# Performance work log

Hardware: AMD Instinct MI355X
Metric: run time of the kernel (lower is better)

Reference implementation:

```python
import jax, jax.numpy as jnp
import numpy as np

L, N, D = 4, 50000, 64        # lookback, n_nodes, gnn_dim
E = 500000                    # n_edges
HID = 256
LN_EPS = 1e-5


def setup_inputs() -> dict:
    key = jax.random.key(0)
    ks = jax.random.split(key, 8)
    h_all = jax.random.normal(ks[0], (L, N, D), dtype=jnp.float32)
    src = jax.random.randint(ks[1], (E,), 0, N, dtype=jnp.int32)
    dst = jax.random.randint(ks[2], (E,), 0, N, dtype=jnp.int32)
    W1 = jax.random.normal(ks[3], (HID, L * 2 * D), dtype=jnp.float32) * (1.0 / np.sqrt(L * 2 * D))
    b1 = jax.random.normal(ks[4], (HID,), dtype=jnp.float32) * 0.01
    W3 = jax.random.normal(ks[5], (1, HID), dtype=jnp.float32) * (1.0 / np.sqrt(HID))
    b3 = jax.random.normal(ks[6], (1,), dtype=jnp.float32) * 0.01
    gamma2 = jnp.ones((HID,), dtype=jnp.float32)
    beta2 = jnp.zeros((HID,), dtype=jnp.float32)
    return {"h_all": h_all, "src": src, "dst": dst, "W1": W1, "b1": b1,
            "W3": W3, "b3": b3, "gamma2": gamma2, "beta2": beta2}


def reference(h_all, src, dst, W1, b1, W3, b3, gamma2, beta2):
    lb, _, d = h_all.shape
    # importance weights 1..L normalized
    imp = jnp.arange(1, lb + 1, dtype=h_all.dtype)
    imp = imp / imp.sum()
    # per-edge gather of src/dst features for every lookback step: [L, E, 2D]
    hs = h_all[:, src]                                  # [L, E, D]
    hd = h_all[:, dst]                                  # [L, E, D]
    embed = jnp.concatenate([hs, hd], axis=-1) * imp[:, None, None]
    # concat over lookback steps -> [E, L*2D]
    embed = jnp.transpose(embed, (1, 0, 2)).reshape(embed.shape[1], -1)
    # MLP: W1(tanh) -> LayerNorm -> dropout(eval=identity) -> relu -> W3
    x = jnp.tanh(embed) @ W1.T + b1                     # [E, HID]
    mu = jnp.mean(x, axis=-1, keepdims=True)
    var = jnp.var(x, axis=-1, keepdims=True)
    x = (x - mu) * jax.lax.rsqrt(var + LN_EPS) * gamma2 + beta2
    x = jax.nn.relu(x)
    out = x @ W3.T + b3                                 # [E, 1]
    return out[:, 0]
```

## Files before the change

kernel.cpp:

```cpp
#include <hip/hip_runtime.h>
#include <hip/hip_bf16.h>

#define LL 4
#define NN 50000
#define DD 64
#define EE 500000
#define HID 256
#define KDIM 512
#define LN_EPS 1e-5f

typedef __bf16 bf16x8 __attribute__((ext_vector_type(8)));
typedef float f32x16 __attribute__((ext_vector_type(16)));

__device__ __forceinline__ void async16(const void* g, void* l) {
    __builtin_amdgcn_global_load_lds(
        (const __attribute__((address_space(1))) void*)g,
        (__attribute__((address_space(3))) void*)l, 16, 0, 0);
}

__global__ void w2_conv(const float* __restrict__ w1, __bf16* __restrict__ o) {
    int t = blockIdx.x * 256 + threadIdx.x;
    int j  = t & 511;
    int b  = t >> 9;
    int k0 = (b >> 1) * 16 + (b & 1) * 8;
    int r  = j & 255;
    int col = (k0 >> 6) * 128 + ((j >> 8) ? 64 : 0) + (k0 & 63);
    const float4* p = (const float4*)(w1 + r * KDIM + col);
    float4 va = p[0];
    float4 vb = p[1];
    bf16x8 v;
    v[0] = (__bf16)va.x; v[1] = (__bf16)va.y; v[2] = (__bf16)va.z; v[3] = (__bf16)va.w;
    v[4] = (__bf16)vb.x; v[5] = (__bf16)vb.y; v[6] = (__bf16)vb.z; v[7] = (__bf16)vb.w;
    *(bf16x8*)(o + (size_t)t * 8) = v;
}

__global__ __launch_bounds__(256, 4)
void node_proj(const float* __restrict__ h, const __bf16* __restrict__ w2c,
               const float* __restrict__ b1, __bf16* __restrict__ P) {
    __shared__ __align__(16) __bf16 Bs[2][16384];

    const int tid  = threadIdx.x;
    const int wave = tid >> 6;
    const int lane = tid & 63;
    const int h32  = lane >> 5;
    const int c32  = lane & 31;
    const int n00  = blockIdx.x * 128;

    #pragma unroll
    for (int it = 0; it < 8; ++it) {
        int o = it * 2048 + tid * 8;
        async16(w2c + (size_t)(o >> 9) * 4096 + (o & 511), &Bs[0][o]);
    }

    int node = n00 + wave * 32 + c32;
    if (node >= NN) node = NN - 1;
    bf16x8 af[16];
    #pragma unroll
    for (int u = 0; u < 16; ++u) {
        int l = u >> 2;
        float imp = (float)(l + 1) * 0.1f;
        const float* p = h + (size_t)l * (NN * DD) + node * DD
                       + (u & 3) * 16 + h32 * 8;
        float4 va = *(const float4*)p;
        float4 vb = *(const float4*)(p + 4);
        float xv[8] = {va.x, va.y, va.z, va.w, vb.x, vb.y, vb.z, vb.w};
        #pragma unroll
        for (int z = 0; z < 8; ++z) {
            float e2 = __expf(2.0f * (imp * xv[z]));
            af[u][z] = (__bf16)(1.0f - 2.0f / (e2 + 1.0f));
        }
    }

    __syncthreads();

    for (int p = 0; p < 8; ++p) {
        const int bp = p & 1;
        if (p < 7) {
            #pragma unroll
            for (int it = 0; it < 8; ++it) {
                int o = it * 2048 + tid * 8;
                async16(w2c + (size_t)(o >> 9) * 4096 + (p + 1) * 512 + (o & 511),
                        &Bs[bp ^ 1][o]);
            }
        }

        f32x16 acc[2];
        acc[0] = (f32x16)(0.f);
        acc[1] = (f32x16)(0.f);
        #pragma unroll
        for (int u = 0; u < 16; ++u) {
            const __bf16* Bk = &Bs[bp][(u * 2 + h32) * 512 + c32 * 8];
            #pragma unroll
            for (int nt = 0; nt < 2; ++nt) {
                bf16x8 bf = *(const bf16x8*)(Bk + nt * 256);
                acc[nt] = __builtin_amdgcn_mfma_f32_32x32x16_bf16(af[u], bf, acc[nt], 0, 0, 0);
            }
        }

        #pragma unroll
        for (int nt = 0; nt < 2; ++nt) {
            int col = p * 64 + nt * 32 + c32;
            float b1v = (col >= 256) ? b1[col - 256] : 0.f;
            #pragma unroll
            for (int r = 0; r < 16; ++r) {
                int row = (r & 3) + 8 * (r >> 2) + 4 * h32;
                int n = n00 + wave * 32 + row;
                if (n < NN)
                    P[(size_t)n * 512 + col] = (__bf16)(acc[nt][r] + b1v);
            }
        }

        __syncthreads();
    }
}

__global__ __launch_bounds__(256, 3)
void edge_out(const __bf16* __restrict__ P, const int* __restrict__ src,
              const int* __restrict__ dst,
              const float* __restrict__ w3, const float* __restrict__ b3,
              const float* __restrict__ gamma, const float* __restrict__ beta,
              float* __restrict__ out) {
    const int tid = threadIdx.x;
    const int g   = tid >> 4;
    const int j   = tid & 15;

    float gv[16], btv[16], wv[16];
    {
        const float4* pg = (const float4*)(gamma + j * 16);
        const float4* pt = (const float4*)(beta + j * 16);
        const float4* pw = (const float4*)(w3 + j * 16);
        #pragma unroll
        for (int z = 0; z < 4; ++z) {
            float4 vg = pg[z], vt = pt[z], vw = pw[z];
            gv [z*4+0] = vg.x; gv [z*4+1] = vg.y; gv [z*4+2] = vg.z; gv [z*4+3] = vg.w;
            btv[z*4+0] = vt.x; btv[z*4+1] = vt.y; btv[z*4+2] = vt.z; btv[z*4+3] = vt.w;
            wv [z*4+0] = vw.x; wv [z*4+1] = vw.y; wv [z*4+2] = vw.z; wv [z*4+3] = vw.w;
        }
    }
    const float b3v = b3[0];
    const int e0 = blockIdx.x * 128 + g * 8;

    int ep = e0 + (j & 7);
    if (ep >= EE) ep = EE - 1;
    const int sj = src[ep];
    const int dj = dst[ep];

    uint4 s0[3], s1[3], d0[3], d1[3];

    #pragma unroll
    for (int i = 0; i < 2; ++i) {
        int s = __shfl(sj, i, 16);
        int d = __shfl(dj, i, 16);
        const uint4* ps = (const uint4*)(P + (size_t)s * 512 + j * 16);
        const uint4* pd = (const uint4*)(P + (size_t)d * 512 + 256 + j * 16);
        s0[i] = ps[0]; s1[i] = ps[1]; d0[i] = pd[0]; d1[i] = pd[1];
    }

    #pragma unroll
    for (int i = 0; i < 8; ++i) {
        if (i + 2 < 8) {
            const int slot = (i + 2) % 3;
            int s = __shfl(sj, i + 2, 16);
            int d = __shfl(dj, i + 2, 16);
            const uint4* ps = (const uint4*)(P + (size_t)s * 512 + j * 16);
            const uint4* pd = (const uint4*)(P + (size_t)d * 512 + 256 + j * 16);
            s0[slot] = ps[0]; s1[slot] = ps[1]; d0[slot] = pd[0]; d1[slot] = pd[1];
        }
        const int cs = i % 3;
        bf16x8 a0 = __builtin_bit_cast(bf16x8, s0[cs]);
        bf16x8 a1 = __builtin_bit_cast(bf16x8, s1[cs]);
        bf16x8 c0 = __builtin_bit_cast(bf16x8, d0[cs]);
        bf16x8 c1 = __builtin_bit_cast(bf16x8, d1[cs]);
        float x[16];
        #pragma unroll
        for (int z = 0; z < 8; ++z) {
            x[z]     = (float)a0[z] + (float)c0[z];
            x[z + 8] = (float)a1[z] + (float)c1[z];
        }
        float sum = 0.f, sq = 0.f;
        #pragma unroll
        for (int z = 0; z < 16; ++z) {
            sum += x[z];
            sq   = fmaf(x[z], x[z], sq);
        }
        #pragma unroll
        for (int m = 1; m < 16; m <<= 1) {
            sum += __shfl_xor(sum, m);
            sq  += __shfl_xor(sq,  m);
        }
        float mu = sum * (1.0f / 256.0f);
        float rs = rsqrtf(sq * (1.0f / 256.0f) - mu * mu + LN_EPS);
        float dot = 0.f;
        #pragma unroll
        for (int z = 0; z < 16; ++z) {
            float y = fmaxf((x[z] - mu) * rs * gv[z] + btv[z], 0.f);
            dot = fmaf(y, wv[z], dot);
        }
        #pragma unroll
        for (int m = 1; m < 16; m <<= 1) dot += __shfl_xor(dot, m);
        int e = e0 + i;
        if (j == 0 && e < EE) out[e] = dot + b3v;
        cs0: ;
    }

    #pragma unroll
    for (int z = 0; z < 16; ++z)
        asm volatile("" :: "v"(gv[z]), "v"(btv[z]), "v"(wv[z]));
}

extern "C" void kernel_launch(void* const* d_in, const int* in_sizes, int n_in,
                              void* d_out, int out_size, void* d_ws, size_t ws_size,
                              hipStream_t stream) {
    const float* h_all  = (const float*)d_in[0];
    const int*   src    = (const int*)  d_in[1];
    const int*   dst    = (const int*)  d_in[2];
    const float* W1     = (const float*)d_in[3];
    const float* b1     = (const float*)d_in[4];
    const float* W3     = (const float*)d_in[5];
    const float* b3     = (const float*)d_in[6];
    const float* gamma2 = (const float*)d_in[7];
    const float* beta2  = (const float*)d_in[8];
    float* out = (float*)d_out;

    __bf16* w2c = (__bf16*)d_ws;
    __bf16* P   = w2c + 131072;

    w2_conv<<<64, 256, 0, stream>>>(W1, w2c);
    node_proj<<<(NN + 127) / 128, 256, 0, stream>>>(h_all, w2c, b1, P);
    edge_out<<<(EE + 127) / 128, 256, 0, stream>>>(P, src, dst, W3, b3,
                                                   gamma2, beta2, out);
}
```

Baseline: 216.7 us.

## Stage node_proj output through LDS for coalesced 16-byte stores, wider N tiles

The node projection kernel now computes 128 output columns per pass instead of 64, with one 64KB LDS buffer replacing the double buffer. Results are staged in LDS and written to P as coalesced 16-byte vectors rather than scattered 2-byte stores. The cost is losing the overlap of weight prefetch with compute, adding extra barriers, and using more LDS, so occupancy drops (launch bounds 4 to 2).

New measurement: 194.1 us, median of 2. -10.5%, faster.

```diff
diff --git a/kernel.cpp b/kernel.cpp
--- a/kernel.cpp
+++ b/kernel.cpp
@@ -34,10 +34,12 @@
     *(bf16x8*)(o + (size_t)t * 8) = v;
 }
 
-__global__ __launch_bounds__(256, 4)
+__global__ __launch_bounds__(256, 2)
 void node_proj(const float* __restrict__ h, const __bf16* __restrict__ w2c,
                const float* __restrict__ b1, __bf16* __restrict__ P) {
-    __shared__ __align__(16) __bf16 Bs[2][16384];
+    __shared__ __align__(16) char smem[65536];
+    __bf16* Bs  = (__bf16*)smem;
+    __bf16* Cs2 = (__bf16*)smem;
 
     const int tid  = threadIdx.x;
     const int wave = tid >> 6;
@@ -47,9 +49,9 @@
     const int n00  = blockIdx.x * 128;
 
     #pragma unroll
-    for (int it = 0; it < 8; ++it) {
+    for (int it = 0; it < 16; ++it) {
         int o = it * 2048 + tid * 8;
-        async16(w2c + (size_t)(o >> 9) * 4096 + (o & 511), &Bs[0][o]);
+        async16(w2c + (size_t)(o >> 10) * 4096 + (o & 1023), Bs + o);
     }
 
     int node = n00 + wave * 32 + c32;
@@ -71,46 +73,58 @@
         }
     }
 
-    __syncthreads();
-
-    for (int p = 0; p < 8; ++p) {
-        const int bp = p & 1;
-        if (p < 7) {
+    for (int cb = 0; cb < 4; ++cb) {
+        __syncthreads();
+
+        f32x16 acc[4];
+        #pragma unroll
+        for (int nt = 0; nt < 4; ++nt) acc[nt] = (f32x16)(0.f);
+
+        #pragma unroll
+        for (int u = 0; u < 16; ++u) {
+            const __bf16* Bk = Bs + (u * 2 + h32) * 1024 + c32 * 8;
             #pragma unroll
-            for (int it = 0; it < 8; ++it) {
-                int o = it * 2048 + tid * 8;
-                async16(w2c + (size_t)(o >> 9) * 4096 + (p + 1) * 512 + (o & 511),
-                        &Bs[bp ^ 1][o]);
-            }
-        }
-
-        f32x16 acc[2];
-        acc[0] = (f32x16)(0.f);
-        acc[1] = (f32x16)(0.f);
-        #pragma unroll
-        for (int u = 0; u < 16; ++u) {
-            const __bf16* Bk = &Bs[bp][(u * 2 + h32) * 512 + c32 * 8];
-            #pragma unroll
-            for (int nt = 0; nt < 2; ++nt) {
+            for (int nt = 0; nt < 4; ++nt) {
                 bf16x8 bf = *(const bf16x8*)(Bk + nt * 256);
                 acc[nt] = __builtin_amdgcn_mfma_f32_32x32x16_bf16(af[u], bf, acc[nt], 0, 0, 0);
             }
         }
-
-        #pragma unroll
-        for (int nt = 0; nt < 2; ++nt) {
-            int col = p * 64 + nt * 32 + c32;
-            float b1v = (col >= 256) ? b1[col - 256] : 0.f;
+        __syncthreads();
+
+        float b1v[4];
+        #pragma unroll
+        for (int nt = 0; nt < 4; ++nt)
+            b1v[nt] = (cb >= 2) ? b1[(cb - 2) * 128 + nt * 32 + c32] : 0.f;
+
+        #pragma unroll
+        for (int nt = 0; nt < 4; ++nt) {
             #pragma unroll
             for (int r = 0; r < 16; ++r) {
-                int row = (r & 3) + 8 * (r >> 2) + 4 * h32;
-                int n = n00 + wave * 32 + row;
-                if (n < NN)
-                    P[(size_t)n * 512 + col] = (__bf16)(acc[nt][r] + b1v);
+                int nl = wave * 32 + (r & 3) + 8 * (r >> 2) + 4 * h32;
+                Cs2[nl * 128 + nt * 32 + c32] = (__bf16)(acc[nt][r] + b1v[nt]);
             }
         }
-
         __syncthreads();
+
+        #pragma unroll
+        for (int it = 0; it < 8; ++it) {
+            int o  = it * 2048 + tid * 8;
+            int nl = o >> 7;
+            int n  = n00 + nl;
+            if (n < NN)
+                *(bf16x8*)(P + (size_t)n * 512 + cb * 128 + (o & 127)) =
+                    *(const bf16x8*)(Cs2 + o);
+        }
+
+        if (cb < 3) {
+            __syncthreads();
+            #pragma unroll
+            for (int it = 0; it < 16; ++it) {
+                int o = it * 2048 + tid * 8;
+                async16(w2c + (size_t)(o >> 10) * 4096 + (cb + 1) * 1024 + (o & 1023),
+                        Bs + o);
+            }
+        }
     }
 }
 
@@ -200,7 +214,6 @@
         for (int m = 1; m < 16; m <<= 1) dot += __shfl_xor(dot, m);
         int e = e0 + i;
         if (j == 0 && e < EE) out[e] = dot + b3v;
-        cs0: ;
     }
 
     #pragma unroll
```
